# Kernel optimization log

Hardware: AMD Instinct MI355X
Metric: run time of the kernel (lower is better)

Reference implementation:

```python
import jax, jax.numpy as jnp
import numpy as np

D_EMB = 2048
N_HEADS = 16
D_K = D_EMB // N_HEADS  # 128
MAX_LEN = 128           # must equal D_K for the (faithful) buggy mask broadcast
VOCAB = 30000
N_LAYERS = 6
BATCH = 8
SEQ = 128
D_FF = 4 * D_EMB


def _sinusoidal_pe(length, d):
    pos = jnp.arange(length, dtype=jnp.float32)[:, None]
    div = jnp.exp(-jnp.log(10000.0) * jnp.arange(0, d, 2, dtype=jnp.float32) / d)
    pe = jnp.zeros((length, d), dtype=jnp.float32)
    pe = pe.at[:, 0::2].set(jnp.sin(pos * div))
    pe = pe.at[:, 1::2].set(jnp.cos(pos * div))
    return pe


def _layernorm(x, g, b, eps=1e-5):
    m = jnp.mean(x, axis=-1, keepdims=True)
    v = jnp.var(x, axis=-1, keepdims=True)
    return g * (x - m) * jax.lax.rsqrt(v + eps) + b


def _attention(x, ctx, Wq, Wk, Wv, Wo, mask):
    # Faithful to source: reshape [B,L,H,dk] then swap LAST TWO axes -> [B,L,dk,H],
    # so scores are [B,L,dk,dk] (attention over the d_k axis, per token).
    B, L, D = x.shape
    split = lambda t: t.reshape(B, L, N_HEADS, D_K).swapaxes(-2, -1)  # [B,L,dk,H]
    Q = split(x @ Wq.T)
    K = split(ctx @ Wk.T)
    V = split(ctx @ Wv.T)
    qk = (Q @ K.swapaxes(-2, -1)) / np.sqrt(D_K)  # [B,L,dk,dk]
    if mask is not None:
        qk = qk + mask  # mask [L,L] broadcasts (L == dk == max_len)
    attn = jax.nn.softmax(qk, axis=-1) @ V        # [B,L,dk,H]
    concat = attn.swapaxes(-2, -1).reshape(B, L, D)
    return concat @ Wo.T


def _decoder(x, context, params):
    p = params
    L = x.shape[1]
    x = x + _sinusoidal_pe(L, D_EMB)
    mask = jnp.triu(jnp.full((L, L), -jnp.inf, dtype=x.dtype), k=1)
    for _ in range(N_LAYERS):  # weights are SHARED across layers (as in source)
        x = _layernorm(_attention(x, x, p['Wq1'], p['Wk1'], p['Wv1'], p['Wo1'], mask),
                       p['g1'], p['be1'])
        x = _layernorm(_attention(x, context, p['Wq2'], p['Wk2'], p['Wv2'], p['Wo2'], None),
                       p['g2'], p['be2'])
        h = jax.nn.relu(x @ p['W_ff1'].T + p['b_ff1']) @ p['W_ff2'].T + p['b_ff2']
        x = _layernorm(h, p['g3'], p['be3'])
    logits = (x @ p['W_lin'].T + p['b_lin']) / 1.0  # temperature = 1.0
    # Faithful to source: softmax over dim=1 (sequence axis), then take last batch element
    return jax.nn.softmax(logits, axis=1)[-1]  # [L, VOCAB]


def setup_inputs() -> dict:
    key = jax.random.key(0)
    ks = jax.random.split(key, 20)
    a = np.sqrt(3.0 / D_EMB)
    u = lambda k, sh: jax.random.uniform(k, sh, jnp.float32, -a, a)
    inp = {
        'x': jax.random.normal(ks[0], (BATCH, SEQ, D_EMB), jnp.float32),
        'context': jax.random.normal(ks[1], (BATCH, SEQ, D_EMB), jnp.float32),
        'Wq1': u(ks[2], (D_EMB, D_EMB)), 'Wk1': u(ks[3], (D_EMB, D_EMB)),
        'Wv1': u(ks[4], (D_EMB, D_EMB)), 'Wo1': u(ks[5], (D_EMB, D_EMB)),
        'Wq2': u(ks[6], (D_EMB, D_EMB)), 'Wk2': u(ks[7], (D_EMB, D_EMB)),
        'Wv2': u(ks[8], (D_EMB, D_EMB)), 'Wo2': u(ks[9], (D_EMB, D_EMB)),
        'W_ff1': u(ks[10], (D_FF, D_EMB)), 'b_ff1': jnp.zeros((D_FF,), jnp.float32),
        'W_ff2': jax.random.uniform(ks[11], (D_EMB, D_FF), jnp.float32, -np.sqrt(1.0 / D_FF), np.sqrt(1.0 / D_FF)),
        'b_ff2': jnp.zeros((D_EMB,), jnp.float32),
        'g1': jnp.ones((D_EMB,), jnp.float32), 'be1': jnp.zeros((D_EMB,), jnp.float32),
        'g2': jnp.ones((D_EMB,), jnp.float32), 'be2': jnp.zeros((D_EMB,), jnp.float32),
        'g3': jnp.ones((D_EMB,), jnp.float32), 'be3': jnp.zeros((D_EMB,), jnp.float32),
        'W_lin': u(ks[12], (VOCAB, D_EMB)), 'b_lin': jnp.zeros((VOCAB,), jnp.float32),
    }
    return inp


def reference(x, context, Wq1, Wk1, Wv1, Wo1, Wq2, Wk2, Wv2, Wo2,
              W_ff1, b_ff1, W_ff2, b_ff2, g1, be1, g2, be2, g3, be3,
              W_lin, b_lin):
    params = dict(Wq1=Wq1, Wk1=Wk1, Wv1=Wv1, Wo1=Wo1,
                  Wq2=Wq2, Wk2=Wk2, Wv2=Wv2, Wo2=Wo2,
                  W_ff1=W_ff1, b_ff1=b_ff1, W_ff2=W_ff2, b_ff2=b_ff2,
                  g1=g1, be1=be1, g2=g2, be2=be2, g3=g3, be3=be3,
                  W_lin=W_lin, b_lin=b_lin)
    return _decoder(x, context, params)
```

## Files before the change

### kernel.cpp

```cpp
#include <hip/hip_runtime.h>
#include <hip/hip_bf16.h>
#include <math.h>

#define D_EMB 2048
#define NH 16
#define DK 128
#define SEQN 128
#define DFF 8192
#define VOCAB 30000
#define NLAYERS 6
#define TOKF (SEQN * D_EMB)

typedef __attribute__((ext_vector_type(8))) short short8v;
typedef __attribute__((ext_vector_type(4))) float float4v;
typedef __hip_bfloat16 bf16;

#define GLOAD_LDS16(g, l)                                                      \
    __builtin_amdgcn_global_load_lds(                                          \
        (const __attribute__((address_space(1))) void*)(g),                    \
        (__attribute__((address_space(3))) void*)(l), 16, 0, 0)

#define WAIT_BAR(n)                                                            \
    do {                                                                       \
        asm volatile("s_waitcnt vmcnt(" #n ")" ::: "memory");                  \
        __builtin_amdgcn_s_barrier();                                          \
        asm volatile("" ::: "memory");                                         \
    } while (0)

struct CvtArgs {
    const float* src[8];
    bf16* dst[8];
};

__global__ __launch_bounds__(256) void cvt_kernel(CvtArgs args, int n4) {
    int i = blockIdx.x * 256 + threadIdx.x;
    if (i >= n4) return;
    const float4* s = (const float4*)args.src[blockIdx.z];
    float4 v = s[i];
    union { short4 s4; bf16 h[4]; } u;
    u.h[0] = __float2bfloat16(v.x);
    u.h[1] = __float2bfloat16(v.y);
    u.h[2] = __float2bfloat16(v.z);
    u.h[3] = __float2bfloat16(v.w);
    ((short4*)args.dst[blockIdx.z])[i] = u.s4;
}

__global__ __launch_bounds__(256) void add_pe_kernel(const float* __restrict__ x,
                                                     bf16* __restrict__ out) {
    int idx = blockIdx.x * 256 + threadIdx.x;
    int l = idx >> 11;
    int d = idx & 2047;
    float two_i = (float)(d & ~1);
    float div = __expf(-9.210340371976184f * two_i * (1.0f / 2048.0f));
    float ang = (float)l * div;
    float pe = (d & 1) ? cosf(ang) : sinf(ang);
    out[idx] = __float2bfloat16(x[(size_t)7 * SEQN * D_EMB + idx] + pe);
}

__global__ __launch_bounds__(256) void gemm_mfma_kernel(
    const bf16* __restrict__ A,
    const bf16* B0, const bf16* B1, const bf16* B2,
    const float* bias0, const float* bias1, const float* bias2,
    void* C0, void* C1, void* C2,
    int M, int N, int K, int relu, int out_bf16, int ksplit, int kslog)
{
    int nwg = gridDim.x * gridDim.y * gridDim.z;
    int orig = blockIdx.x + gridDim.x * (blockIdx.y + gridDim.y * blockIdx.z);
    int wg = orig;
    if ((nwg & 7) == 0) wg = (orig & 7) * (nwg >> 3) + (orig >> 3);
    int bx = wg % gridDim.x;
    int t1 = wg / gridDim.x;
    int by = t1 % gridDim.y;
    int bz = t1 / gridDim.y;

    int oi = bz >> kslog;
    int kh = bz & (ksplit - 1);
    int kbase = kh << 9;

    const bf16* B    = (oi == 0) ? B0    : (oi == 1) ? B1    : B2;
    const float* bias = (oi == 0) ? bias0 : (oi == 1) ? bias1 : bias2;
    void* C          = (oi == 0) ? C0    : (oi == 1) ? C1    : C2;

    __shared__ __align__(16) bf16 As[4][64 * 128];
    __shared__ __align__(16) bf16 Bs[4][64 * 128];

    int tid = threadIdx.x;
    int w = tid >> 6;
    int lane = tid & 63;
    int m0 = bx * 64;
    int n0 = by * 64;
    int wm = (w & 1) * 32;
    int wn = (w >> 1) * 32;
    int fcol = lane & 15;
    int fqu  = lane >> 4;
    int rr   = (w << 2) + (lane >> 4);
    int scol = lane & 15;

    float4v acc[2][2];
    acc[0][0] = (float4v)0.0f; acc[0][1] = (float4v)0.0f;
    acc[1][0] = (float4v)0.0f; acc[1][1] = (float4v)0.0f;

    #pragma unroll
    for (int c = 0; c < 4; ++c) {
        const bf16* a0 = A + (size_t)m0 * K + kbase + (c << 7);
        const bf16* b0 = B + (size_t)n0 * K + kbase + (c << 7);
        #pragma unroll
        for (int t = 0; t < 4; ++t) {
            int r = t * 16 + rr;
            int s = scol ^ (r & 15);
            GLOAD_LDS16(a0 + (size_t)r * K + s * 8,
                        (char*)As[c] + (size_t)(t * 16 + (w << 2)) * 256);
            GLOAD_LDS16(b0 + (size_t)r * K + s * 8,
                        (char*)Bs[c] + (size_t)(t * 16 + (w << 2)) * 256);
        }
    }

    auto compute_chunk = [&](int c) {
        #pragma unroll
        for (int kk = 0; kk < 4; ++kk) {
            short8v a[2], b[2];
            int slog = kk * 4 + fqu;
            #pragma unroll
            for (int fm = 0; fm < 2; ++fm) {
                int m = wm + fm * 16 + fcol;
                a[fm] = *(const short8v*)((const char*)As[c] + m * 256 + ((slog ^ (m & 15)) << 4));
            }
            #pragma unroll
            for (int fn = 0; fn < 2; ++fn) {
                int n = wn + fn * 16 + fcol;
                b[fn] = *(const short8v*)((const char*)Bs[c] + n * 256 + ((slog ^ (n & 15)) << 4));
            }
            #pragma unroll
            for (int fm = 0; fm < 2; ++fm)
                #pragma unroll
                for (int fn = 0; fn < 2; ++fn)
                    acc[fm][fn] = __builtin_amdgcn_mfma_f32_16x16x32_bf16(
                        a[fm], b[fn], acc[fm][fn], 0, 0, 0);
        }
    };

    WAIT_BAR(24); compute_chunk(0);
    WAIT_BAR(16); compute_chunk(1);
    WAIT_BAR(8);  compute_chunk(2);
    WAIT_BAR(0);  compute_chunk(3);

    int rbase = fqu * 4;
    #pragma unroll
    for (int fm = 0; fm < 2; ++fm) {
        #pragma unroll
        for (int fn = 0; fn < 2; ++fn) {
            int n = n0 + wn + fn * 16 + fcol;
            #pragma unroll
            for (int r = 0; r < 4; ++r) {
                int m = m0 + wm + fm * 16 + rbase + r;
                float v = acc[fm][fn][r];
                if (out_bf16) {
                    v += bias ? bias[n] : 0.0f;
                    if (relu) v = fmaxf(v, 0.0f);
                    ((bf16*)C)[(size_t)m * N + n] = __float2bfloat16(v);
                } else {
                    ((float*)C)[(size_t)kh * M * N + (size_t)m * N + n] = v;
                }
            }
        }
    }
}

__global__ __launch_bounds__(256) void biasrelu_kernel(
    const float* __restrict__ P, const float* __restrict__ bias,
    bf16* __restrict__ H)
{
    int i4 = blockIdx.x * 256 + threadIdx.x;
    const size_t n4 = (size_t)SEQN * DFF / 4;
    const float4* p = (const float4*)P;
    float4 v0 = p[i4];
    float4 v1 = p[i4 + n4];
    float4 v2 = p[i4 + 2 * n4];
    float4 v3 = p[i4 + 3 * n4];
    float4 b4 = ((const float4*)bias)[i4 & (DFF / 4 - 1)];
    union { short4 s4; bf16 h[4]; } u;
    u.h[0] = __float2bfloat16(fmaxf(v0.x + v1.x + v2.x + v3.x + b4.x, 0.0f));
    u.h[1] = __float2bfloat16(fmaxf(v0.y + v1.y + v2.y + v3.y + b4.y, 0.0f));
    u.h[2] = __float2bfloat16(fmaxf(v0.z + v1.z + v2.z + v3.z + b4.z, 0.0f));
    u.h[3] = __float2bfloat16(fmaxf(v0.w + v1.w + v2.w + v3.w + b4.w, 0.0f));
    ((short4*)H)[i4] = u.s4;
}

__global__ __launch_bounds__(256) void attn_token_kernel(
    const float* __restrict__ qp,
    const float* __restrict__ kp, const float* __restrict__ vp,
    bf16* __restrict__ O, int causal, int qparts, int kvparts)
{
    int l = blockIdx.x;
    int tid = threadIdx.x;
    int i = tid & 127;
    int half = tid >> 7;
    __shared__ __align__(16) float qs[D_EMB];
    __shared__ __align__(16) float ks[D_EMB];
    __shared__ __align__(16) float vs[D_EMB];
    __shared__ float m1s[128], l1s[128];
    __shared__ float acc1s[128][NH + 1];
    size_t base = (size_t)l * D_EMB;

    for (int d4 = tid; d4 < D_EMB / 4; d4 += 256) {
        float4 q = {0.0f, 0.0f, 0.0f, 0.0f};
        for (int p = 0; p < qparts; ++p) {
            float4 t = ((const float4*)(qp + (size_t)p * TOKF + base))[d4];
            q.x += t.x; q.y += t.y; q.z += t.z; q.w += t.w;
        }
        ((float4*)qs)[d4] = q;
        float4 kv = {0.0f, 0.0f, 0.0f, 0.0f}, vv = {0.0f, 0.0f, 0.0f, 0.0f};
        for (int p = 0; p < kvparts; ++p) {
            float4 t = ((const float4*)(kp + (size_t)p * TOKF + base))[d4];
            kv.x += t.x; kv.y += t.y; kv.z += t.z; kv.w += t.w;
            float4 s = ((const float4*)(vp + (size_t)p * TOKF + base))[d4];
            vv.x += s.x; vv.y += s.y; vv.z += s.z; vv.w += s.w;
        }
        ((float4*)ks)[d4] = kv;
        ((float4*)vs)[d4] = vv;
    }
    __syncthreads();

    const float scale = 0.088388347648318447f;
    float qr[NH];
    #pragma unroll
    for (int h = 0; h < NH; ++h) qr[h] = qs[h * DK + i];

    int jmax = causal ? (i + 1) : DK;
    int j0 = half * 64;
    int j1 = (jmax < j0 + 64) ? jmax : (j0 + 64);

    float m = -INFINITY, lsum = 0.0f;
    float acc[NH];
    #pragma unroll
    for (int h = 0; h < NH; ++h) acc[h] = 0.0f;

    for (int j = j0; j < j1; j += 4) {
        float4 s4 = {0.0f, 0.0f, 0.0f, 0.0f};
        #pragma unroll
        for (int h = 0; h < NH; ++h) {
            float4 kv = *(const float4*)&ks[h * DK + j];
            s4.x += qr[h] * kv.x; s4.y += qr[h] * kv.y;
            s4.z += qr[h] * kv.z; s4.w += qr[h] * kv.w;
        }
        float sv0 = s4.x * scale;
        float sv1 = (j + 1 < j1) ? s4.y * scale : -INFINITY;
        float sv2 = (j + 2 < j1) ? s4.z * scale : -INFINITY;
        float sv3 = (j + 3 < j1) ? s4.w * scale : -INFINITY;
        float mx = fmaxf(fmaxf(sv0, sv1), fmaxf(sv2, sv3));
        float nm = fmaxf(m, mx);
        float f  = __expf(m - nm);
        float p0 = __expf(sv0 - nm);
        float p1 = __expf(sv1 - nm);
        float p2 = __expf(sv2 - nm);
        float p3 = __expf(sv3 - nm);
        lsum = lsum * f + ((p0 + p1) + (p2 + p3));
        #pragma unroll
        for (int h = 0; h < NH; ++h) {
            float4 vv = *(const float4*)&vs[h * DK + j];
            acc[h] = acc[h] * f + ((p0 * vv.x + p1 * vv.y) + (p2 * vv.z + p3 * vv.w));
        }
        m = nm;
    }

    if (half) {
        m1s[i] = m; l1s[i] = lsum;
        #pragma unroll
        for (int h = 0; h < NH; ++h) acc1s[i][h] = acc[h];
    }
    __syncthreads();
    if (!half) {
        float m1 = m1s[i], l1 = l1s[i];
        float nm = fmaxf(m, m1);
        float f0 = __expf(m - nm);
        float f1 = __expf(m1 - nm);
        float rinv = 1.0f / (lsum * f0 + l1 * f1);
        #pragma unroll
        for (int h = 0; h < NH; ++h)
            O[base + h * DK + i] =
                __float2bfloat16((acc[h] * f0 + acc1s[i][h] * f1) * rinv);
    }
}

__global__ __launch_bounds__(256) void layernorm_kernel(
    const float* __restrict__ pa, int nparts,
    const float* __restrict__ addb,
    const float* __restrict__ g, const float* __restrict__ b,
    bf16* __restrict__ Y)
{
    int row = blockIdx.x;
    size_t base = (size_t)row * D_EMB;
    __shared__ __align__(16) float4 vs4[D_EMB / 4];
    __shared__ float buf[256];
    int tid = threadIdx.x;

    float s = 0.0f;
    for (int d4 = tid; d4 < D_EMB / 4; d4 += 256) {
        float4 v = {0.0f, 0.0f, 0.0f, 0.0f};
        if (addb) v = ((const float4*)addb)[d4];
        for (int p = 0; p < nparts; ++p) {
            float4 t = ((const float4*)(pa + (size_t)p * TOKF + base))[d4];
            v.x += t.x; v.y += t.y; v.z += t.z; v.w += t.w;
        }
        vs4[d4] = v;
        s += (v.x + v.y) + (v.z + v.w);
    }
    buf[tid] = s; __syncthreads();
    for (int off = 128; off; off >>= 1) {
        if (tid < off) buf[tid] += buf[tid + off];
        __syncthreads();
    }
    float mean = buf[0] * (1.0f / D_EMB);
    __syncthreads();

    float vsum = 0.0f;
    for (int d4 = tid; d4 < D_EMB / 4; d4 += 256) {
        float4 v = vs4[d4];
        float t0 = v.x - mean, t1 = v.y - mean, t2 = v.z - mean, t3 = v.w - mean;
        vsum += (t0 * t0 + t1 * t1) + (t2 * t2 + t3 * t3);
    }
    buf[tid] = vsum; __syncthreads();
    for (int off = 128; off; off >>= 1) {
        if (tid < off) buf[tid] += buf[tid + off];
        __syncthreads();
    }
    float inv = rsqrtf(buf[0] * (1.0f / D_EMB) + 1e-5f);

    for (int d4 = tid; d4 < D_EMB / 4; d4 += 256) {
        float4 v = vs4[d4];
        float4 g4 = ((const float4*)g)[d4];
        float4 b4 = ((const float4*)b)[d4];
        union { short4 s4; bf16 h[4]; } u;
        u.h[0] = __float2bfloat16(g4.x * (v.x - mean) * inv + b4.x);
        u.h[1] = __float2bfloat16(g4.y * (v.y - mean) * inv + b4.y);
        u.h[2] = __float2bfloat16(g4.z * (v.z - mean) * inv + b4.z);
        u.h[3] = __float2bfloat16(g4.w * (v.w - mean) * inv + b4.w);
        ((short4*)(Y + base))[d4] = u.s4;
    }
}

__global__ __launch_bounds__(256) void logits_softmax_kernel(
    const bf16* __restrict__ X, const float* __restrict__ W,
    float* __restrict__ out)
{
    __shared__ __align__(16) bf16 As[128 * 128];
    __shared__ __align__(16) bf16 Bs[64 * 128];
    __shared__ float red[4][64];

    int tid = threadIdx.x;
    int w = tid >> 6;
    int lane = tid & 63;
    int fcol = lane & 15;
    int fqu  = lane >> 4;
    int n0 = blockIdx.x * 64;

    float4v acc[2][4];
    #pragma unroll
    for (int fm = 0; fm < 2; ++fm)
        #pragma unroll
        for (int fn = 0; fn < 4; ++fn) acc[fm][fn] = (float4v)0.0f;

    int brow = tid >> 2;
    int q    = tid & 3;
    int gn   = n0 + brow;

    for (int k0 = 0; k0 < D_EMB; k0 += 128) {
        #pragma unroll
        for (int t = 0; t < 8; ++t) {
            int r = t * 16 + (w << 2) + (lane >> 4);
            int s = (lane & 15) ^ (r & 15);
            GLOAD_LDS16(X + (size_t)r * D_EMB + k0 + s * 8,
                        (char*)As + (size_t)(t * 16 + (w << 2)) * 256);
        }
        #pragma unroll
        for (int j = 0; j < 4; ++j) {
            int sL = q * 4 + j;
            union { short8v v; bf16 h[8]; } u;
            if (gn < VOCAB) {
                const float* gp = W + (size_t)gn * D_EMB + k0 + sL * 8;
                float4 f0 = *(const float4*)gp;
                float4 f1 = *(const float4*)(gp + 4);
                u.h[0] = __float2bfloat16(f0.x); u.h[1] = __float2bfloat16(f0.y);
                u.h[2] = __float2bfloat16(f0.z); u.h[3] = __float2bfloat16(f0.w);
                u.h[4] = __float2bfloat16(f1.x); u.h[5] = __float2bfloat16(f1.y);
                u.h[6] = __float2bfloat16(f1.z); u.h[7] = __float2bfloat16(f1.w);
            } else {
                u.v = (short8v)0;
            }
            *(short8v*)((char*)Bs + brow * 256 + ((sL ^ (brow & 15)) << 4)) = u.v;
        }
        __syncthreads();

        #pragma unroll
        for (int kk = 0; kk < 4; ++kk) {
            int slog = kk * 4 + fqu;
            short8v a[2], b[4];
            #pragma unroll
            for (int fm = 0; fm < 2; ++fm) {
                int m = w * 32 + fm * 16 + fcol;
                a[fm] = *(const short8v*)((const char*)As + m * 256 + ((slog ^ (m & 15)) << 4));
            }
            #pragma unroll
            for (int fn = 0; fn < 4; ++fn) {
                int n = fn * 16 + fcol;
                b[fn] = *(const short8v*)((const char*)Bs + n * 256 + ((slog ^ (n & 15)) << 4));
            }
            #pragma unroll
            for (int fm = 0; fm < 2; ++fm)
                #pragma unroll
                for (int fn = 0; fn < 4; ++fn)
                    acc[fm][fn] = __builtin_amdgcn_mfma_f32_16x16x32_bf16(
                        a[fm], b[fn], acc[fm][fn], 0, 0, 0);
        }
        __syncthreads();
    }

    float cmax[4];
    #pragma unroll
    for (int fn = 0; fn < 4; ++fn) {
        float m = -INFINITY;
        #pragma unroll
        for (int fm = 0; fm < 2; ++fm)
            #pragma unroll
            for (int r = 0; r < 4; ++r) m = fmaxf(m, acc[fm][fn][r]);
        m = fmaxf(m, __shfl_xor(m, 16));
        m = fmaxf(m, __shfl_xor(m, 32));
        cmax[fn] = m;
    }
    if (lane < 16) {
        #pragma unroll
        for (int fn = 0; fn < 4; ++fn) red[w][fn * 16 + lane] = cmax[fn];
    }
    __syncthreads();
    #pragma unroll
    for (int fn = 0; fn < 4; ++fn) {
        float m = red[0][fn * 16 + fcol];
        m = fmaxf(m, red[1][fn * 16 + fcol]);
// ... 20 lines not shown
        csum[fn] = s;
    }
    if (lane < 16) {
        #pragma unroll
        for (int fn = 0; fn < 4; ++fn) red[w][fn * 16 + lane] = csum[fn];
    }
    __syncthreads();
    #pragma unroll
    for (int fn = 0; fn < 4; ++fn) {
        float s = red[0][fn * 16 + fcol] + red[1][fn * 16 + fcol]
                + red[2][fn * 16 + fcol] + red[3][fn * 16 + fcol];
        float rinv = 1.0f / s;
        int c = n0 + fn * 16 + fcol;
        if (c < VOCAB) {
            #pragma unroll
            for (int fm = 0; fm < 2; ++fm)
                #pragma unroll
                for (int r = 0; r < 4; ++r) {
                    int rw = w * 32 + fm * 16 + fqu * 4 + r;
                    out[(size_t)rw * VOCAB + c] = acc[fm][fn][r] * rinv;
                }
        }
    }
}

static inline void launch_gemm(const bf16* A,
                               const bf16* B0, const bf16* B1, const bf16* B2,
                               const float* bias0, const float* bias1, const float* bias2,
                               void* C0, void* C1, void* C2,
                               int M, int N, int K, int relu, int out_bf16,
                               int nout, hipStream_t s)
{
    int ksplit = K >> 9;
    int kslog = (ksplit == 4) ? 2 : (ksplit == 16) ? 4 : (ksplit == 8) ? 3 : 0;
    dim3 grid(M / 64, N / 64, nout * ksplit);
    hipLaunchKernelGGL(gemm_mfma_kernel, grid, dim3(256), 0, s,
                       A, B0, B1, B2, bias0, bias1, bias2, C0, C1, C2,
                       M, N, K, relu, out_bf16, ksplit, kslog);
}

extern "C" void kernel_launch(void* const* d_in, const int* in_sizes, int n_in,
                              void* d_out, int out_size, void* d_ws, size_t ws_size,
                              hipStream_t stream)
{
    const float* x_in   = (const float*)d_in[0];
    const float* ctx_in = (const float*)d_in[1];
    const float* Wq1 = (const float*)d_in[2];
    const float* Wk1 = (const float*)d_in[3];
    const float* Wv1 = (const float*)d_in[4];
    const float* Wo1 = (const float*)d_in[5];
    const float* Wq2 = (const float*)d_in[6];
    const float* Wk2 = (const float*)d_in[7];
    const float* Wv2 = (const float*)d_in[8];
    const float* Wo2 = (const float*)d_in[9];
    const float* W_ff1 = (const float*)d_in[10];
    const float* b_ff1 = (const float*)d_in[11];
    const float* W_ff2 = (const float*)d_in[12];
    const float* b_ff2 = (const float*)d_in[13];
    const float* g1  = (const float*)d_in[14];
    const float* be1 = (const float*)d_in[15];
    const float* g2  = (const float*)d_in[16];
    const float* be2 = (const float*)d_in[17];
    const float* g3  = (const float*)d_in[18];
    const float* be3 = (const float*)d_in[19];
    const float* W_lin = (const float*)d_in[20];
    float* out = (float*)d_out;

    const size_t W2 = (size_t)D_EMB * D_EMB;
    const size_t WF = (size_t)DFF * D_EMB;

    char* p = (char*)d_ws;
    bf16* wq1 = (bf16*)p; p += W2 * 2;
    bf16* wk1 = (bf16*)p; p += W2 * 2;
    bf16* wv1 = (bf16*)p; p += W2 * 2;
    bf16* wo1 = (bf16*)p; p += W2 * 2;
    bf16* wq2 = (bf16*)p; p += W2 * 2;
    bf16* wk2 = (bf16*)p; p += W2 * 2;
    bf16* wv2 = (bf16*)p; p += W2 * 2;
    bf16* wo2 = (bf16*)p; p += W2 * 2;
    bf16* wff1 = (bf16*)p; p += WF * 2;
    bf16* wff2 = (bf16*)p; p += WF * 2;
    bf16* wctx = (bf16*)p; p += (size_t)TOKF * 2;
    bf16* X    = (bf16*)p; p += (size_t)TOKF * 2;
    bf16* Att  = (bf16*)p; p += (size_t)TOKF * 2;
    bf16* H    = (bf16*)p; p += (size_t)SEQN * DFF * 2;
    float* Qp  = (float*)p; p += (size_t)4 * TOKF * 4;
    float* Kp  = (float*)p; p += (size_t)4 * TOKF * 4;
    float* Vp  = (float*)p; p += (size_t)4 * TOKF * 4;
    float* X2p = (float*)p; p += (size_t)16 * TOKF * 4;
    float* K2p = (float*)p; p += (size_t)4 * TOKF * 4;
    float* V2p = (float*)p; p += (size_t)4 * TOKF * 4;
    float* FFp = (float*)p; p += (size_t)4 * SEQN * DFF * 4;

    const float* ctx7 = ctx_in + (size_t)7 * SEQN * D_EMB;

    {
        CvtArgs a = {};
        a.src[0] = Wq1; a.dst[0] = wq1;  a.src[1] = Wk1; a.dst[1] = wk1;
        a.src[2] = Wv1; a.dst[2] = wv1;  a.src[3] = Wo1; a.dst[3] = wo1;
        a.src[4] = Wq2; a.dst[4] = wq2;  a.src[5] = Wk2; a.dst[5] = wk2;
        a.src[6] = Wv2; a.dst[6] = wv2;  a.src[7] = Wo2; a.dst[7] = wo2;
        int n4 = (int)(W2 / 4);
        hipLaunchKernelGGL(cvt_kernel, dim3((n4 + 255) / 256, 1, 8), dim3(256), 0,
                           stream, a, n4);
    }
    {
        CvtArgs a = {};
        a.src[0] = W_ff1; a.dst[0] = wff1;
        a.src[1] = W_ff2; a.dst[1] = wff2;
        int n4 = (int)(WF / 4);
        hipLaunchKernelGGL(cvt_kernel, dim3((n4 + 255) / 256, 1, 2), dim3(256), 0,
                           stream, a, n4);
    }
    {
        CvtArgs a = {};
        a.src[0] = ctx7; a.dst[0] = wctx;
        int n4 = TOKF / 4;
        hipLaunchKernelGGL(cvt_kernel, dim3((n4 + 255) / 256, 1, 1), dim3(256), 0,
                           stream, a, n4);
    }

    hipLaunchKernelGGL(add_pe_kernel, dim3((SEQN * D_EMB) / 256), dim3(256), 0,
                       stream, x_in, X);

    launch_gemm(wctx, wk2, wv2, wv2, nullptr, nullptr, nullptr,
                K2p, V2p, V2p, SEQN, D_EMB, D_EMB, 0, 0, 2, stream);

    for (int layer = 0; layer < NLAYERS; ++layer) {
        launch_gemm(X, wq1, wk1, wv1, nullptr, nullptr, nullptr,
                    Qp, Kp, Vp, SEQN, D_EMB, D_EMB, 0, 0, 3, stream);
        hipLaunchKernelGGL(attn_token_kernel, dim3(SEQN), dim3(256), 0, stream,
                           Qp, Kp, Vp, Att, 1, 4, 4);
        launch_gemm(Att, wo1, wo1, wo1, nullptr, nullptr, nullptr,
                    X2p, X2p, X2p, SEQN, D_EMB, D_EMB, 0, 0, 1, stream);
        hipLaunchKernelGGL(layernorm_kernel, dim3(SEQN), dim3(256), 0, stream,
                           X2p, 4, (const float*)nullptr, g1, be1, X);

        launch_gemm(X, wq2, wq2, wq2, nullptr, nullptr, nullptr,
                    Qp, Qp, Qp, SEQN, D_EMB, D_EMB, 0, 0, 1, stream);
        hipLaunchKernelGGL(attn_token_kernel, dim3(SEQN), dim3(256), 0, stream,
                           Qp, K2p, V2p, Att, 0, 4, 4);
        launch_gemm(Att, wo2, wo2, wo2, nullptr, nullptr, nullptr,
                    X2p, X2p, X2p, SEQN, D_EMB, D_EMB, 0, 0, 1, stream);
        hipLaunchKernelGGL(layernorm_kernel, dim3(SEQN), dim3(256), 0, stream,
                           X2p, 4, (const float*)nullptr, g2, be2, X);

        launch_gemm(X, wff1, wff1, wff1, nullptr, nullptr, nullptr,
                    FFp, FFp, FFp, SEQN, DFF, D_EMB, 0, 0, 1, stream);
        hipLaunchKernelGGL(biasrelu_kernel, dim3((SEQN * DFF / 4) / 256), dim3(256),
                           0, stream, FFp, b_ff1, H);
        launch_gemm(H, wff2, wff2, wff2, nullptr, nullptr, nullptr,
                    X2p, X2p, X2p, SEQN, D_EMB, DFF, 0, 0, 1, stream);
        hipLaunchKernelGGL(layernorm_kernel, dim3(SEQN), dim3(256), 0, stream,
                           X2p, 16, b_ff2, g3, be3, X);
    }

    hipLaunchKernelGGL(logits_softmax_kernel, dim3((VOCAB + 63) / 64), dim3(256),
                       0, stream, X, W_lin, out);
}
```

Measured before the change: 1.437 ms.

## Fuse all decoder stages into one persistent kernel with grid barriers

Replaces the sequence of separate kernel launches (conversions, PE add, GEMMs, attention, layernorms, bias-relu, logits) with one persistent mega kernel. Phases are separated by a software grid-wide barrier built on atomics. The grid size comes from occupancy and is capped at 256 blocks. Work is distributed by a job loop, and the logits weight loads are register-prefetched. This removes launch overhead and inter-kernel gaps for about 60 small launches, and lets the next layer's QKV GEMM follow directly. In exchange it adds spin-barrier cost, limits concurrency to co-resident blocks, and risks deadlock if not all blocks are resident.

```diff
diff --git a/kernel.cpp b/kernel.cpp
--- a/kernel.cpp
+++ b/kernel.cpp
@@ -27,68 +27,90 @@
         asm volatile("" ::: "memory");                                         \
     } while (0)
 
-struct CvtArgs {
-    const float* src[8];
-    bf16* dst[8];
+struct MegaArgs {
+    const float *x7, *ctx7;
+    const float *Wq1, *Wk1, *Wv1, *Wo1, *Wq2, *Wk2, *Wv2, *Wo2;
+    const float *W_ff1, *b_ff1, *W_ff2, *b_ff2;
+    const float *g1, *be1, *g2, *be2, *g3, *be3;
+    const float *W_lin;
+    float *out;
+    bf16 *wq1, *wk1, *wv1, *wo1, *wq2, *wk2, *wv2, *wo2, *wff1, *wff2, *wctx;
+    bf16 *X, *Att, *H;
+    float *Qp, *Kp, *Vp, *X2p, *K2p, *V2p, *FFp;
 };
 
-__global__ __launch_bounds__(256) void cvt_kernel(CvtArgs args, int n4) {
-    int i = blockIdx.x * 256 + threadIdx.x;
-    if (i >= n4) return;
-    const float4* s = (const float4*)args.src[blockIdx.z];
-    float4 v = s[i];
+__device__ __forceinline__ void gsync(unsigned* cnt, unsigned* gen) {
+    __syncthreads();
+    if (threadIdx.x == 0) {
+        __threadfence();
+        unsigned g = __hip_atomic_load(gen, __ATOMIC_RELAXED, __HIP_MEMORY_SCOPE_AGENT);
+        unsigned nblk = gridDim.x;
+        if (__hip_atomic_fetch_add(cnt, 1u, __ATOMIC_ACQ_REL, __HIP_MEMORY_SCOPE_AGENT)
+            == nblk - 1u) {
+            __hip_atomic_store(cnt, 0u, __ATOMIC_RELAXED, __HIP_MEMORY_SCOPE_AGENT);
+            __hip_atomic_store(gen, g + 1u, __ATOMIC_RELEASE, __HIP_MEMORY_SCOPE_AGENT);
+        } else {
+            while (__hip_atomic_load(gen, __ATOMIC_RELAXED, __HIP_MEMORY_SCOPE_AGENT) == g)
+                __builtin_amdgcn_s_sleep(8);
+        }
+        __threadfence();
+    }
+    __syncthreads();
+}
+
+__device__ __forceinline__ short4 pack4(float a, float b, float c, float d) {
     union { short4 s4; bf16 h[4]; } u;
-    u.h[0] = __float2bfloat16(v.x);
-    u.h[1] = __float2bfloat16(v.y);
-    u.h[2] = __float2bfloat16(v.z);
-    u.h[3] = __float2bfloat16(v.w);
-    ((short4*)args.dst[blockIdx.z])[i] = u.s4;
-}
-
-__global__ __launch_bounds__(256) void add_pe_kernel(const float* __restrict__ x,
-                                                     bf16* __restrict__ out) {
-    int idx = blockIdx.x * 256 + threadIdx.x;
-    int l = idx >> 11;
-    int d = idx & 2047;
-    float two_i = (float)(d & ~1);
-    float div = __expf(-9.210340371976184f * two_i * (1.0f / 2048.0f));
-    float ang = (float)l * div;
-    float pe = (d & 1) ? cosf(ang) : sinf(ang);
-    out[idx] = __float2bfloat16(x[(size_t)7 * SEQN * D_EMB + idx] + pe);
-}
-
-__global__ __launch_bounds__(256) void gemm_mfma_kernel(
-    const bf16* __restrict__ A,
-    const bf16* B0, const bf16* B1, const bf16* B2,
-    const float* bias0, const float* bias1, const float* bias2,
-    void* C0, void* C1, void* C2,
-    int M, int N, int K, int relu, int out_bf16, int ksplit, int kslog)
-{
-    int nwg = gridDim.x * gridDim.y * gridDim.z;
-    int orig = blockIdx.x + gridDim.x * (blockIdx.y + gridDim.y * blockIdx.z);
-    int wg = orig;
-    if ((nwg & 7) == 0) wg = (orig & 7) * (nwg >> 3) + (orig >> 3);
-    int bx = wg % gridDim.x;
-    int t1 = wg / gridDim.x;
-    int by = t1 % gridDim.y;
-    int bz = t1 / gridDim.y;
-
-    int oi = bz >> kslog;
-    int kh = bz & (ksplit - 1);
-    int kbase = kh << 9;
-
-    const bf16* B    = (oi == 0) ? B0    : (oi == 1) ? B1    : B2;
-    const float* bias = (oi == 0) ? bias0 : (oi == 1) ? bias1 : bias2;
-    void* C          = (oi == 0) ? C0    : (oi == 1) ? C1    : C2;
-
-    __shared__ __align__(16) bf16 As[4][64 * 128];
-    __shared__ __align__(16) bf16 Bs[4][64 * 128];
+    u.h[0] = __float2bfloat16(a); u.h[1] = __float2bfloat16(b);
+    u.h[2] = __float2bfloat16(c); u.h[3] = __float2bfloat16(d);
+    return u.s4;
+}
+
+__device__ void cvt_seg(const float* __restrict__ src, bf16* __restrict__ dst,
+                        int n4, int gid, int gstride) {
+    const float4* s = (const float4*)src;
+    short4* d = (short4*)dst;
+    int i = gid;
+    for (; i + 3 * gstride < n4; i += 4 * gstride) {
+        float4 v0 = s[i];
+        float4 v1 = s[i + gstride];
+        float4 v2 = s[i + 2 * gstride];
+        float4 v3 = s[i + 3 * gstride];
+        d[i]               = pack4(v0.x, v0.y, v0.z, v0.w);
+        d[i + gstride]     = pack4(v1.x, v1.y, v1.z, v1.w);
+        d[i + 2 * gstride] = pack4(v2.x, v2.y, v2.z, v2.w);
+        d[i + 3 * gstride] = pack4(v3.x, v3.y, v3.z, v3.w);
+    }
+    for (; i < n4; i += gstride) {
+        float4 v = s[i];
+        d[i] = pack4(v.x, v.y, v.z, v.w);
+    }
+}
+
+__device__ void pe_seg(const float* __restrict__ x7, bf16* __restrict__ X,
+                       int gid, int gstride) {
+    for (int i4 = gid; i4 < TOKF / 4; i4 += gstride) {
+        int idx = i4 << 2;
+        int l = idx >> 11;
+        int d = idx & 2047;
+        float4 xv = ((const float4*)x7)[i4];
+        float div0 = __expf(-9.210340371976184f * ((float)d * (1.0f / 2048.0f)));
+        float div1 = __expf(-9.210340371976184f * ((float)(d + 2) * (1.0f / 2048.0f)));
+        float a0 = (float)l * div0, a1 = (float)l * div1;
+        ((short4*)X)[i4] = pack4(xv.x + sinf(a0), xv.y + cosf(a0),
+                                 xv.z + sinf(a1), xv.w + cosf(a1));
+    }
+}
+
+__device__ __forceinline__ void gemm_job(char* smem, const bf16* __restrict__ A,
+                                         const bf16* __restrict__ B,
+                                         float* __restrict__ C,
+                                         int N, int K, int kbase, int m0, int n0) {
+    char* AsB = smem;
+    char* BsB = smem + 65536;
 
     int tid = threadIdx.x;
     int w = tid >> 6;
     int lane = tid & 63;
-    int m0 = bx * 64;
-    int n0 = by * 64;
     int wm = (w & 1) * 32;
     int wn = (w >> 1) * 32;
     int fcol = lane & 15;
@@ -109,13 +131,15 @@
             int r = t * 16 + rr;
             int s = scol ^ (r & 15);
             GLOAD_LDS16(a0 + (size_t)r * K + s * 8,
-                        (char*)As[c] + (size_t)(t * 16 + (w << 2)) * 256);
+                        AsB + (size_t)c * 16384 + (size_t)(t * 16 + (w << 2)) * 256);
             GLOAD_LDS16(b0 + (size_t)r * K + s * 8,
-                        (char*)Bs[c] + (size_t)(t * 16 + (w << 2)) * 256);
+                        BsB + (size_t)c * 16384 + (size_t)(t * 16 + (w << 2)) * 256);
         }
     }
 
     auto compute_chunk = [&](int c) {
+        const char* Ac = AsB + (size_t)c * 16384;
+        const char* Bc = BsB + (size_t)c * 16384;
         #pragma unroll
         for (int kk = 0; kk < 4; ++kk) {
             short8v a[2], b[2];
@@ -123,12 +147,12 @@
             #pragma unroll
             for (int fm = 0; fm < 2; ++fm) {
                 int m = wm + fm * 16 + fcol;
-                a[fm] = *(const short8v*)((const char*)As[c] + m * 256 + ((slog ^ (m & 15)) << 4));
+                a[fm] = *(const short8v*)(Ac + m * 256 + ((slog ^ (m & 15)) << 4));
             }
             #pragma unroll
             for (int fn = 0; fn < 2; ++fn) {
                 int n = wn + fn * 16 + fcol;
-                b[fn] = *(const short8v*)((const char*)Bs[c] + n * 256 + ((slog ^ (n & 15)) << 4));
+                b[fn] = *(const short8v*)(Bc + n * 256 + ((slog ^ (n & 15)) << 4));
             }
             #pragma unroll
             for (int fm = 0; fm < 2; ++fm)
@@ -146,76 +170,66 @@
 
     int rbase = fqu * 4;
     #pragma unroll
-    for (int fm = 0; fm < 2; ++fm) {
+    for (int fm = 0; fm < 2; ++fm)
         #pragma unroll
         for (int fn = 0; fn < 2; ++fn) {
             int n = n0 + wn + fn * 16 + fcol;
             #pragma unroll
             for (int r = 0; r < 4; ++r) {
                 int m = m0 + wm + fm * 16 + rbase + r;
-                float v = acc[fm][fn][r];
-                if (out_bf16) {
-                    v += bias ? bias[n] : 0.0f;
-                    if (relu) v = fmaxf(v, 0.0f);
-                    ((bf16*)C)[(size_t)m * N + n] = __float2bfloat16(v);
-                } else {
-                    ((float*)C)[(size_t)kh * M * N + (size_t)m * N + n] = v;
-                }
-            }
-        }
-    }
-}
-
-__global__ __launch_bounds__(256) void biasrelu_kernel(
-    const float* __restrict__ P, const float* __restrict__ bias,
-    bf16* __restrict__ H)
-{
-    int i4 = blockIdx.x * 256 + threadIdx.x;
-    const size_t n4 = (size_t)SEQN * DFF / 4;
-    const float4* p = (const float4*)P;
-    float4 v0 = p[i4];
-    float4 v1 = p[i4 + n4];
-    float4 v2 = p[i4 + 2 * n4];
-    float4 v3 = p[i4 + 3 * n4];
-    float4 b4 = ((const float4*)bias)[i4 & (DFF / 4 - 1)];
-    union { short4 s4; bf16 h[4]; } u;
-    u.h[0] = __float2bfloat16(fmaxf(v0.x + v1.x + v2.x + v3.x + b4.x, 0.0f));
-    u.h[1] = __float2bfloat16(fmaxf(v0.y + v1.y + v2.y + v3.y + b4.y, 0.0f));
-    u.h[2] = __float2bfloat16(fmaxf(v0.z + v1.z + v2.z + v3.z + b4.z, 0.0f));
-    u.h[3] = __float2bfloat16(fmaxf(v0.w + v1.w + v2.w + v3.w + b4.w, 0.0f));
-    ((short4*)H)[i4] = u.s4;
-}
-
-__global__ __launch_bounds__(256) void attn_token_kernel(
-    const float* __restrict__ qp,
-    const float* __restrict__ kp, const float* __restrict__ vp,
-    bf16* __restrict__ O, int causal, int qparts, int kvparts)
-{
-    int l = blockIdx.x;
+                C[(size_t)m * N + n] = acc[fm][fn][r];
+            }
+        }
+    __syncthreads();
+}
+
+__device__ void gemm_phase(char* smem, const bf16* A,
+                           const bf16* B0, const bf16* B1, const bf16* B2,
+                           float* C0, float* C1, float* C2,
+                           int M, int N, int K, int kslog, int nout,
+                           int bid, int nblk) {
+    int MB = M >> 6, NB = N >> 6;
+    int ksplit = 1 << kslog;
+    int njobs = MB * NB * nout * ksplit;
+    for (int job = bid; job < njobs; job += nblk) {
+        int bx = job % MB;
+        int r1 = job / MB;
+        int by = r1 % NB;
+        int bz = r1 / NB;
+        int oi = bz >> kslog;
+        int kh = bz & (ksplit - 1);
+        const bf16* B = (oi == 0) ? B0 : (oi == 1) ? B1 : B2;
+        float* C = (oi == 0) ? C0 : (oi == 1) ? C1 : C2;
+        gemm_job(smem, A, B, C + (size_t)kh * M * N, N, K, kh << 9, bx << 6, by << 6);
+    }
+}
+
+__device__ void attn_job(char* smem, const float* __restrict__ qp,
+                         const float* __restrict__ kp, const float* __restrict__ vp,
+                         bf16* __restrict__ O, int causal, int l) {
     int tid = threadIdx.x;
     int i = tid & 127;
     int half = tid >> 7;
-    __shared__ __align__(16) float qs[D_EMB];
-    __shared__ __align__(16) float ks[D_EMB];
-    __shared__ __align__(16) float vs[D_EMB];
-    __shared__ float m1s[128], l1s[128];
-    __shared__ float acc1s[128][NH + 1];
+    float* qs = (float*)smem;
+    float* ks = qs + D_EMB;
+    float* vs = ks + D_EMB;
+    float* m1s = vs + D_EMB;
+    float* l1s = m1s + 128;
+    float (*acc1s)[NH + 1] = (float(*)[NH + 1])(l1s + 128);
     size_t base = (size_t)l * D_EMB;
 
     for (int d4 = tid; d4 < D_EMB / 4; d4 += 256) {
-        float4 q = {0.0f, 0.0f, 0.0f, 0.0f};
-        for (int p = 0; p < qparts; ++p) {
+        float4 q = {0, 0, 0, 0}, kv = {0, 0, 0, 0}, vv = {0, 0, 0, 0};
+        #pragma unroll
+        for (int p = 0; p < 4; ++p) {
             float4 t = ((const float4*)(qp + (size_t)p * TOKF + base))[d4];
             q.x += t.x; q.y += t.y; q.z += t.z; q.w += t.w;
-        }
-        ((float4*)qs)[d4] = q;
-        float4 kv = {0.0f, 0.0f, 0.0f, 0.0f}, vv = {0.0f, 0.0f, 0.0f, 0.0f};
-        for (int p = 0; p < kvparts; ++p) {
-            float4 t = ((const float4*)(kp + (size_t)p * TOKF + base))[d4];
-            kv.x += t.x; kv.y += t.y; kv.z += t.z; kv.w += t.w;
+            float4 u = ((const float4*)(kp + (size_t)p * TOKF + base))[d4];
+            kv.x += u.x; kv.y += u.y; kv.z += u.z; kv.w += u.w;
             float4 s = ((const float4*)(vp + (size_t)p * TOKF + base))[d4];
             vv.x += s.x; vv.y += s.y; vv.z += s.z; vv.w += s.w;
         }
+        ((float4*)qs)[d4] = q;
         ((float4*)ks)[d4] = kv;
         ((float4*)vs)[d4] = vv;
     }
@@ -236,7 +250,7 @@
     for (int h = 0; h < NH; ++h) acc[h] = 0.0f;
 
     for (int j = j0; j < j1; j += 4) {
-        float4 s4 = {0.0f, 0.0f, 0.0f, 0.0f};
+        float4 s4 = {0, 0, 0, 0};
         #pragma unroll
         for (int h = 0; h < NH; ++h) {
             float4 kv = *(const float4*)&ks[h * DK + j];
@@ -280,26 +294,25 @@
             O[base + h * DK + i] =
                 __float2bfloat16((acc[h] * f0 + acc1s[i][h] * f1) * rinv);
     }
-}
-
-__global__ __launch_bounds__(256) void layernorm_kernel(
-    const float* __restrict__ pa, int nparts,
-    const float* __restrict__ addb,
-    const float* __restrict__ g, const float* __restrict__ b,
-    bf16* __restrict__ Y)
-{
-    int row = blockIdx.x;
+    __syncthreads();
+}
+
+template<int NPARTS>
+__device__ void ln_job(char* smem, const float* __restrict__ parts,
+                       const float* __restrict__ addb, const float* __restrict__ g,
+                       const float* __restrict__ b, bf16* __restrict__ Y, int row) {
+    float4* vs4 = (float4*)smem;
+    float* buf = (float*)(smem + 8192);
+    int tid = threadIdx.x;
     size_t base = (size_t)row * D_EMB;
-    __shared__ __align__(16) float4 vs4[D_EMB / 4];
-    __shared__ float buf[256];
-    int tid = threadIdx.x;
 
     float s = 0.0f;
     for (int d4 = tid; d4 < D_EMB / 4; d4 += 256) {
-        float4 v = {0.0f, 0.0f, 0.0f, 0.0f};
+        float4 v = {0, 0, 0, 0};
         if (addb) v = ((const float4*)addb)[d4];
-        for (int p = 0; p < nparts; ++p) {
-            float4 t = ((const float4*)(pa + (size_t)p * TOKF + base))[d4];
+        #pragma unroll
+        for (int p = 0; p < NPARTS; ++p) {
+            float4 t = ((const float4*)(parts + (size_t)p * TOKF + base))[d4];
             v.x += t.x; v.y += t.y; v.z += t.z; v.w += t.w;
         }
         vs4[d4] = v;
@@ -330,29 +343,43 @@
         float4 v = vs4[d4];
         float4 g4 = ((const float4*)g)[d4];
         float4 b4 = ((const float4*)b)[d4];
-        union { short4 s4; bf16 h[4]; } u;
-        u.h[0] = __float2bfloat16(g4.x * (v.x - mean) * inv + b4.x);
-        u.h[1] = __float2bfloat16(g4.y * (v.y - mean) * inv + b4.y);
-        u.h[2] = __float2bfloat16(g4.z * (v.z - mean) * inv + b4.z);
-        u.h[3] = __float2bfloat16(g4.w * (v.w - mean) * inv + b4.w);
-        ((short4*)(Y + base))[d4] = u.s4;
-    }
-}
-
-__global__ __launch_bounds__(256) void logits_softmax_kernel(
-    const bf16* __restrict__ X, const float* __restrict__ W,
-    float* __restrict__ out)
-{
-    __shared__ __align__(16) bf16 As[128 * 128];
-    __shared__ __align__(16) bf16 Bs[64 * 128];
-    __shared__ float red[4][64];
+        ((short4*)(Y + base))[d4] = pack4(g4.x * (v.x - mean) * inv + b4.x,
+                                          g4.y * (v.y - mean) * inv + b4.y,
+                                          g4.z * (v.z - mean) * inv + b4.z,
+                                          g4.w * (v.w - mean) * inv + b4.w);
+    }
+    __syncthreads();
+}
+
+__device__ void biasrelu_phase(const float* __restrict__ P, const float* __restrict__ bias,
+                               bf16* __restrict__ H, int gid, int gstride) {
+    const int n4 = SEQN * DFF / 4;
+    const float4* p = (const float4*)P;
+    for (int i4 = gid; i4 < n4; i4 += gstride) {
+        float4 v0 = p[i4];
+        float4 v1 = p[i4 + n4];
+        float4 v2 = p[i4 + 2 * n4];
+        float4 v3 = p[i4 + 3 * n4];
+        float4 b4 = ((const float4*)bias)[i4 & (DFF / 4 - 1)];
+        ((short4*)H)[i4] = pack4(fmaxf(v0.x + v1.x + v2.x + v3.x + b4.x, 0.0f),
+                                 fmaxf(v0.y + v1.y + v2.y + v3.y + b4.y, 0.0f),
+                                 fmaxf(v0.z + v1.z + v2.z + v3.z + b4.z, 0.0f),
+                                 fmaxf(v0.w + v1.w + v2.w + v3.w + b4.w, 0.0f));
+    }
+}
+
+__device__ void logits_job(char* smem, const bf16* __restrict__ X,
+                           const float* __restrict__ W, float* __restrict__ out,
+                           int n0) {
+    char* AsB = smem;
+    char* BsB = smem + 32768;
+    float (*red)[64] = (float(*)[64])(smem + 49152);
 
     int tid = threadIdx.x;
     int w = tid >> 6;
     int lane = tid & 63;
     int fcol = lane & 15;
     int fqu  = lane >> 4;
-    int n0 = blockIdx.x * 64;
 
     float4v acc[2][4];
     #pragma unroll
@@ -363,23 +390,36 @@
     int brow = tid >> 2;
     int q    = tid & 3;
     int gn   = n0 + brow;
-
-    for (int k0 = 0; k0 < D_EMB; k0 += 128) {
+    const float* gpbase = W + (size_t)gn * D_EMB;
+
+    float4 wreg[8];
+    auto loadW = [&](int k0) {
+        if (gn < VOCAB) {
+            #pragma unroll
+            for (int j = 0; j < 4; ++j) {
+                const float* gp = gpbase + k0 + (q * 4 + j) * 8;
+                wreg[2 * j]     = *(const float4*)gp;
+                wreg[2 * j + 1] = *(const float4*)(gp + 4);
+            }
+        }
+    };
+    loadW(0);
+
+    for (int k0i = 0; k0i < 16; ++k0i) {
+        int k0 = k0i << 7;
         #pragma unroll
         for (int t = 0; t < 8; ++t) {
             int r = t * 16 + (w << 2) + (lane >> 4);
             int s = (lane & 15) ^ (r & 15);
             GLOAD_LDS16(X + (size_t)r * D_EMB + k0 + s * 8,
-                        (char*)As + (size_t)(t * 16 + (w << 2)) * 256);
+                        AsB + (size_t)(t * 16 + (w << 2)) * 256);
         }
         #pragma unroll
         for (int j = 0; j < 4; ++j) {
             int sL = q * 4 + j;
             union { short8v v; bf16 h[8]; } u;
             if (gn < VOCAB) {
-                const float* gp = W + (size_t)gn * D_EMB + k0 + sL * 8;
-                float4 f0 = *(const float4*)gp;
-                float4 f1 = *(const float4*)(gp + 4);
+                float4 f0 = wreg[2 * j], f1 = wreg[2 * j + 1];
                 u.h[0] = __float2bfloat16(f0.x); u.h[1] = __float2bfloat16(f0.y);
                 u.h[2] = __float2bfloat16(f0.z); u.h[3] = __float2bfloat16(f0.w);
                 u.h[4] = __float2bfloat16(f1.x); u.h[5] = __float2bfloat16(f1.y);
@@ -387,9 +427,16 @@
             } else {
                 u.v = (short8v)0;
             }
-            *(short8v*)((char*)Bs + brow * 256 + ((sL ^ (brow & 15)) << 4)) = u.v;
-        }
-        __syncthreads();
+            *(short8v*)(BsB + brow * 256 + ((sL ^ (brow & 15)) << 4)) = u.v;
+        }
+        if (k0i < 15) {
+            loadW(k0 + 128);
+            asm volatile("s_waitcnt vmcnt(8) lgkmcnt(0)" ::: "memory");
+        } else {
+            asm volatile("s_waitcnt vmcnt(0) lgkmcnt(0)" ::: "memory");
+        }
+        __builtin_amdgcn_s_barrier();
+        asm volatile("" ::: "memory");
 
         #pragma unroll
         for (int kk = 0; kk < 4; ++kk) {
@@ -398,12 +445,12 @@
             #pragma unroll
             for (int fm = 0; fm < 2; ++fm) {
                 int m = w * 32 + fm * 16 + fcol;
-                a[fm] = *(const short8v*)((const char*)As + m * 256 + ((slog ^ (m & 15)) << 4));
+                a[fm] = *(const short8v*)(AsB + m * 256 + ((slog ^ (m & 15)) << 4));
             }
             #pragma unroll
             for (int fn = 0; fn < 4; ++fn) {
                 int n = fn * 16 + fcol;
-                b[fn] = *(const short8v*)((const char*)Bs + n * 256 + ((slog ^ (n & 15)) << 4));
+                b[fn] = *(const short8v*)(BsB + n * 256 + ((slog ^ (n & 15)) << 4));
             }
             #pragma unroll
             for (int fm = 0; fm < 2; ++fm)
@@ -412,7 +459,8 @@
                     acc[fm][fn] = __builtin_amdgcn_mfma_f32_16x16x32_bf16(
                         a[fm], b[fn], acc[fm][fn], 0, 0, 0);
         }
-        __syncthreads();
+        asm volatile("" ::: "memory");
+        __builtin_amdgcn_s_barrier();
     }
 
     float cmax[4];
@@ -479,139 +527,145 @@
                 }
         }
     }
-}
-
-static inline void launch_gemm(const bf16* A,
-                               const bf16* B0, const bf16* B1, const bf16* B2,
-                               const float* bias0, const float* bias1, const float* bias2,
-                               void* C0, void* C1, void* C2,
-                               int M, int N, int K, int relu, int out_bf16,
-                               int nout, hipStream_t s)
-{
-    int ksplit = K >> 9;
-    int kslog = (ksplit == 4) ? 2 : (ksplit == 16) ? 4 : (ksplit == 8) ? 3 : 0;
-    dim3 grid(M / 64, N / 64, nout * ksplit);
-    hipLaunchKernelGGL(gemm_mfma_kernel, grid, dim3(256), 0, s,
-                       A, B0, B1, B2, bias0, bias1, bias2, C0, C1, C2,
-                       M, N, K, relu, out_bf16, ksplit, kslog);
+    __syncthreads();
+}
+
+__global__ __launch_bounds__(256) void mega_kernel(MegaArgs A, unsigned* bcnt,
+                                                   unsigned* bgen) {
+    __shared__ __align__(16) char smem[131072];
+    const int tid = threadIdx.x;
+    const int bid = blockIdx.x;
+    const int nblk = gridDim.x;
+    const int gid = bid * 256 + tid;
+    const int gstride = nblk * 256;
+
+    cvt_seg(A.Wq1, A.wq1, 1048576, gid, gstride);
+    cvt_seg(A.Wk1, A.wk1, 1048576, gid, gstride);
+    cvt_seg(A.Wv1, A.wv1, 1048576, gid, gstride);
+    cvt_seg(A.Wo1, A.wo1, 1048576, gid, gstride);
+    cvt_seg(A.Wq2, A.wq2, 1048576, gid, gstride);
+    cvt_seg(A.Wk2, A.wk2, 1048576, gid, gstride);
+    cvt_seg(A.Wv2, A.wv2, 1048576, gid, gstride);
+    cvt_seg(A.Wo2, A.wo2, 1048576, gid, gstride);
+    cvt_seg(A.W_ff1, A.wff1, 4194304, gid, gstride);
+    cvt_seg(A.W_ff2, A.wff2, 4194304, gid, gstride);
+    cvt_seg(A.ctx7, A.wctx, 65536, gid, gstride);
+    pe_seg(A.x7, A.X, gid, gstride);
+    gsync(bcnt, bgen);
+
+    gemm_phase(smem, A.wctx, A.wk2, A.wv2, A.wv2, A.K2p, A.V2p, A.V2p,
+               SEQN, D_EMB, D_EMB, 2, 2, bid, nblk);
+    gemm_phase(smem, A.X, A.wq1, A.wk1, A.wv1, A.Qp, A.Kp, A.Vp,
+               SEQN, D_EMB, D_EMB, 2, 3, bid, nblk);
+
+    for (int l = 0; l < NLAYERS; ++l) {
+        gsync(bcnt, bgen);
+        for (int j = bid; j < SEQN; j += nblk)
+            attn_job(smem, A.Qp, A.Kp, A.Vp, A.Att, 1, j);
+        gsync(bcnt, bgen);
+        gemm_phase(smem, A.Att, A.wo1, A.wo1, A.wo1, A.X2p, A.X2p, A.X2p,
+                   SEQN, D_EMB, D_EMB, 2, 1, bid, nblk);
+        gsync(bcnt, bgen);
+        for (int j = bid; j < SEQN; j += nblk)
+            ln_job<4>(smem, A.X2p, nullptr, A.g1, A.be1, A.X, j);
+        gsync(bcnt, bgen);
+        gemm_phase(smem, A.X, A.wq2, A.wq2, A.wq2, A.Qp, A.Qp, A.Qp,
+                   SEQN, D_EMB, D_EMB, 2, 1, bid, nblk);
+        gsync(bcnt, bgen);
+        for (int j = bid; j < SEQN; j += nblk)
+            attn_job(smem, A.Qp, A.K2p, A.V2p, A.Att, 0, j);
+        gsync(bcnt, bgen);
+        gemm_phase(smem, A.Att, A.wo2, A.wo2, A.wo2, A.X2p, A.X2p, A.X2p,
+                   SEQN, D_EMB, D_EMB, 2, 1, bid, nblk);
+        gsync(bcnt, bgen);
+        for (int j = bid; j < SEQN; j += nblk)
+            ln_job<4>(smem, A.X2p, nullptr, A.g2, A.be2, A.X, j);
+        gsync(bcnt, bgen);
+        gemm_phase(smem, A.X, A.wff1, A.wff1, A.wff1, A.FFp, A.FFp, A.FFp,
+                   SEQN, DFF, D_EMB, 2, 1, bid, nblk);
+        gsync(bcnt, bgen);
+        biasrelu_phase(A.FFp, A.b_ff1, A.H, gid, gstride);
+        gsync(bcnt, bgen);
+        gemm_phase(smem, A.H, A.wff2, A.wff2, A.wff2, A.X2p, A.X2p, A.X2p,
+                   SEQN, D_EMB, DFF, 4, 1, bid, nblk);
+        gsync(bcnt, bgen);
+        for (int j = bid; j < SEQN; j += nblk)
+            ln_job<16>(smem, A.X2p, A.b_ff2, A.g3, A.be3, A.X, j);
+        gsync(bcnt, bgen);
+        if (l + 1 < NLAYERS)
+            gemm_phase(smem, A.X, A.wq1, A.wk1, A.wv1, A.Qp, A.Kp, A.Vp,
+                       SEQN, D_EMB, D_EMB, 2, 3, bid, nblk);
+    }
+
+    for (int j = bid; j < (VOCAB + 63) / 64; j += nblk)
+        logits_job(smem, A.X, A.W_lin, A.out, j * 64);
 }
 
 extern "C" void kernel_launch(void* const* d_in, const int* in_sizes, int n_in,
                               void* d_out, int out_size, void* d_ws, size_t ws_size,
-                              hipStream_t stream)
-{
+                              hipStream_t stream) {
     const float* x_in   = (const float*)d_in[0];
     const float* ctx_in = (const float*)d_in[1];
-    const float* Wq1 = (const float*)d_in[2];
-    const float* Wk1 = (const float*)d_in[3];
-    const float* Wv1 = (const float*)d_in[4];
-    const float* Wo1 = (const float*)d_in[5];
-    const float* Wq2 = (const float*)d_in[6];
-    const float* Wk2 = (const float*)d_in[7];
-    const float* Wv2 = (const float*)d_in[8];
-    const float* Wo2 = (const float*)d_in[9];
-    const float* W_ff1 = (const float*)d_in[10];
-    const float* b_ff1 = (const float*)d_in[11];
-    const float* W_ff2 = (const float*)d_in[12];
-    const float* b_ff2 = (const float*)d_in[13];
-    const float* g1  = (const float*)d_in[14];
-    const float* be1 = (const float*)d_in[15];
-    const float* g2  = (const float*)d_in[16];
-    const float* be2 = (const float*)d_in[17];
-    const float* g3  = (const float*)d_in[18];
-    const float* be3 = (const float*)d_in[19];
-    const float* W_lin = (const float*)d_in[20];
-    float* out = (float*)d_out;
 
     const size_t W2 = (size_t)D_EMB * D_EMB;
     const size_t WF = (size_t)DFF * D_EMB;
 
-    char* p = (char*)d_ws;
-    bf16* wq1 = (bf16*)p; p += W2 * 2;
-    bf16* wk1 = (bf16*)p; p += W2 * 2;
-    bf16* wv1 = (bf16*)p; p += W2 * 2;
-    bf16* wo1 = (bf16*)p; p += W2 * 2;
-    bf16* wq2 = (bf16*)p; p += W2 * 2;
-    bf16* wk2 = (bf16*)p; p += W2 * 2;
-    bf16* wv2 = (bf16*)p; p += W2 * 2;
-    bf16* wo2 = (bf16*)p; p += W2 * 2;
-    bf16* wff1 = (bf16*)p; p += WF * 2;
-    bf16* wff2 = (bf16*)p; p += WF * 2;
-    bf16* wctx = (bf16*)p; p += (size_t)TOKF * 2;
-    bf16* X    = (bf16*)p; p += (size_t)TOKF * 2;
-    bf16* Att  = (bf16*)p; p += (size_t)TOKF * 2;
-    bf16* H    = (bf16*)p; p += (size_t)SEQN * DFF * 2;
-    float* Qp  = (float*)p; p += (size_t)4 * TOKF * 4;
-    float* Kp  = (float*)p; p += (size_t)4 * TOKF * 4;
-    float* Vp  = (float*)p; p += (size_t)4 * TOKF * 4;
-    float* X2p = (float*)p; p += (size_t)16 * TOKF * 4;
-    float* K2p = (float*)p; p += (size_t)4 * TOKF * 4;
-    float* V2p = (float*)p; p += (size_t)4 * TOKF * 4;
-    float* FFp = (float*)p; p += (size_t)4 * SEQN * DFF * 4;
-
-    const float* ctx7 = ctx_in + (size_t)7 * SEQN * D_EMB;
-
-    {
-        CvtArgs a = {};
-        a.src[0] = Wq1; a.dst[0] = wq1;  a.src[1] = Wk1; a.dst[1] = wk1;
-        a.src[2] = Wv1; a.dst[2] = wv1;  a.src[3] = Wo1; a.dst[3] = wo1;
-        a.src[4] = Wq2; a.dst[4] = wq2;  a.src[5] = Wk2; a.dst[5] = wk2;
-        a.src[6] = Wv2; a.dst[6] = wv2;  a.src[7] = Wo2; a.dst[7] = wo2;
-        int n4 = (int)(W2 / 4);
-        hipLaunchKernelGGL(cvt_kernel, dim3((n4 + 255) / 256, 1, 8), dim3(256), 0,
-                           stream, a, n4);
-    }
-    {
-        CvtArgs a = {};
-        a.src[0] = W_ff1; a.dst[0] = wff1;
-        a.src[1] = W_ff2; a.dst[1] = wff2;
-        int n4 = (int)(WF / 4);
-        hipLaunchKernelGGL(cvt_kernel, dim3((n4 + 255) / 256, 1, 2), dim3(256), 0,
-                           stream, a, n4);
-    }
-    {
-        CvtArgs a = {};
-        a.src[0] = ctx7; a.dst[0] = wctx;
-        int n4 = TOKF / 4;
-        hipLaunchKernelGGL(cvt_kernel, dim3((n4 + 255) / 256, 1, 1), dim3(256), 0,
-                           stream, a, n4);
-    }
-
-    hipLaunchKernelGGL(add_pe_kernel, dim3((SEQN * D_EMB) / 256), dim3(256), 0,
-                       stream, x_in, X);
-
-    launch_gemm(wctx, wk2, wv2, wv2, nullptr, nullptr, nullptr,
-                K2p, V2p, V2p, SEQN, D_EMB, D_EMB, 0, 0, 2, stream);
-
-    for (int layer = 0; layer < NLAYERS; ++layer) {
-        launch_gemm(X, wq1, wk1, wv1, nullptr, nullptr, nullptr,
-                    Qp, Kp, Vp, SEQN, D_EMB, D_EMB, 0, 0, 3, stream);
-        hipLaunchKernelGGL(attn_token_kernel, dim3(SEQN), dim3(256), 0, stream,
-                           Qp, Kp, Vp, Att, 1, 4, 4);
-        launch_gemm(Att, wo1, wo1, wo1, nullptr, nullptr, nullptr,
-                    X2p, X2p, X2p, SEQN, D_EMB, D_EMB, 0, 0, 1, stream);
-        hipLaunchKernelGGL(layernorm_kernel, dim3(SEQN), dim3(256), 0, stream,
-                           X2p, 4, (const float*)nullptr, g1, be1, X);
-
-        launch_gemm(X, wq2, wq2, wq2, nullptr, nullptr, nullptr,
-                    Qp, Qp, Qp, SEQN, D_EMB, D_EMB, 0, 0, 1, stream);
-        hipLaunchKernelGGL(attn_token_kernel, dim3(SEQN), dim3(256), 0, stream,
-                           Qp, K2p, V2p, Att, 0, 4, 4);
-        launch_gemm(Att, wo2, wo2, wo2, nullptr, nullptr, nullptr,
-                    X2p, X2p, X2p, SEQN, D_EMB, D_EMB, 0, 0, 1, stream);
-        hipLaunchKernelGGL(layernorm_kernel, dim3(SEQN), dim3(256), 0, stream,
-                           X2p, 4, (const float*)nullptr, g2, be2, X);
-
-        launch_gemm(X, wff1, wff1, wff1, nullptr, nullptr, nullptr,
-                    FFp, FFp, FFp, SEQN, DFF, D_EMB, 0, 0, 1, stream);
-        hipLaunchKernelGGL(biasrelu_kernel, dim3((SEQN * DFF / 4) / 256), dim3(256),
-                           0, stream, FFp, b_ff1, H);
-        launch_gemm(H, wff2, wff2, wff2, nullptr, nullptr, nullptr,
-                    X2p, X2p, X2p, SEQN, D_EMB, DFF, 0, 0, 1, stream);
-        hipLaunchKernelGGL(layernorm_kernel, dim3(SEQN), dim3(256), 0, stream,
-                           X2p, 16, b_ff2, g3, be3, X);
-    }
-
-    hipLaunchKernelGGL(logits_softmax_kernel, dim3((VOCAB + 63) / 64), dim3(256),
-                       0, stream, X, W_lin, out);
-}
+    unsigned* bcnt = (unsigned*)d_ws;
+    unsigned* bgen = bcnt + 1;
+    char* p = (char*)d_ws + 256;
+
+    MegaArgs a;
+    a.x7   = x_in + (size_t)7 * TOKF;
+    a.ctx7 = ctx_in + (size_t)7 * TOKF;
+    a.Wq1 = (const float*)d_in[2];  a.Wk1 = (const float*)d_in[3];
+    a.Wv1 = (const float*)d_in[4];  a.Wo1 = (const float*)d_in[5];
+    a.Wq2 = (const float*)d_in[6];  a.Wk2 = (const float*)d_in[7];
+    a.Wv2 = (const float*)d_in[8];  a.Wo2 = (const float*)d_in[9];
+    a.W_ff1 = (const float*)d_in[10]; a.b_ff1 = (const float*)d_in[11];
+    a.W_ff2 = (const float*)d_in[12]; a.b_ff2 = (const float*)d_in[13];
+    a.g1 = (const float*)d_in[14]; a.be1 = (const float*)d_in[15];
+    a.g2 = (const float*)d_in[16]; a.be2 = (const float*)d_in[17];
+    a.g3 = (const float*)d_in[18]; a.be3 = (const float*)d_in[19];
+    a.W_lin = (const float*)d_in[20];
+    a.out = (float*)d_out;
+
+    a.wq1 = (bf16*)p; p += W2 * 2;
+    a.wk1 = (bf16*)p; p += W2 * 2;
+    a.wv1 = (bf16*)p; p += W2 * 2;
+    a.wo1 = (bf16*)p; p += W2 * 2;
+    a.wq2 = (bf16*)p; p += W2 * 2;
+    a.wk2 = (bf16*)p; p += W2 * 2;
+    a.wv2 = (bf16*)p; p += W2 * 2;
+    a.wo2 = (bf16*)p; p += W2 * 2;
+    a.wff1 = (bf16*)p; p += WF * 2;
+    a.wff2 = (bf16*)p; p += WF * 2;
+    a.wctx = (bf16*)p; p += (size_t)TOKF * 2;
+    a.X    = (bf16*)p; p += (size_t)TOKF * 2;
+    a.Att  = (bf16*)p; p += (size_t)TOKF * 2;
+    a.H    = (bf16*)p; p += (size_t)SEQN * DFF * 2;
+    a.Qp  = (float*)p; p += (size_t)4 * TOKF * 4;
+    a.Kp  = (float*)p; p += (size_t)4 * TOKF * 4;
+    a.Vp  = (float*)p; p += (size_t)4 * TOKF * 4;
+    a.X2p = (float*)p; p += (size_t)16 * TOKF * 4;
+    a.K2p = (float*)p; p += (size_t)4 * TOKF * 4;
+    a.V2p = (float*)p; p += (size_t)4 * TOKF * 4;
+    a.FFp = (float*)p; p += (size_t)4 * SEQN * DFF * 4;
+
+    static int nblk = 0;
+    if (nblk == 0) {
+        int dev = 0;
+        hipGetDevice(&dev);
+        hipDeviceProp_t prop{};
+        hipGetDeviceProperties(&prop, dev);
+        int maxb = 0;
+        hipOccupancyMaxActiveBlocksPerMultiprocessor(&maxb, mega_kernel, 256, 0);
+        if (maxb < 1) maxb = 1;
+        long cap = (long)prop.multiProcessorCount * maxb;
+        nblk = (int)((cap < 256) ? cap : 256);
+        if (nblk < 1) nblk = 256;
+    }
+
+    hipMemsetAsync(d_ws, 0, 64, stream);
+    hipLaunchKernelGGL(mega_kernel, dim3(nblk), dim3(256), 0, stream,
+                       a, bcnt, bgen);
+}
```

After: 3.483 ms. 2.42x slower.
